# Performance work log

Measured on AMD Instinct MI355X. Metric: run time of the kernel, lower is better.

Reference implementation:

```python
import jax, jax.numpy as jnp
import numpy as np

N, E, EH, RH, R, H = 50000, 800000, 256, 128, 500, 2


def _seg_softmax(e, rel, num_segments):
    # torch_geometric.utils.softmax keyed by rel: (e - max_seg).exp() / (sum_seg + 1e-16)
    m = jax.ops.segment_max(e, rel, num_segments=num_segments)
    m = jnp.where(jnp.isfinite(m), m, 0.0)  # empty segments -> 0
    ex = jnp.exp(e - m[rel])
    s = jax.ops.segment_sum(ex, rel, num_segments=num_segments)
    return ex / (s[rel] + 1e-16)


def setup_inputs() -> dict:
    key = jax.random.key(0)
    ks = jax.random.split(key, 7)
    x_e = jax.random.normal(ks[0], (N, EH), dtype=jnp.float32)
    edge_index = jax.random.randint(ks[1], (2, E), 0, N)
    rel = jax.random.randint(ks[2], (E,), 0, R)
    w_h = jax.random.normal(ks[3], (RH, EH), dtype=jnp.float32) / np.sqrt(EH)
    w_t = jax.random.normal(ks[4], (RH, EH), dtype=jnp.float32) / np.sqrt(EH)
    a_h = jax.random.normal(ks[5], (H, RH), dtype=jnp.float32) / np.sqrt(RH)
    a_t = jax.random.normal(ks[6], (H, RH), dtype=jnp.float32) / np.sqrt(RH)
    return {"x_e": x_e, "edge_index": edge_index, "rel": rel,
            "w_h": w_h, "w_t": w_t, "a_h": a_h, "a_t": a_t, "num_heads": H}


def reference(x_e, edge_index, rel, w_h, w_t, a_h, a_t, num_heads):
    src, dst = edge_index[0], edge_index[1]
    x_r_h = x_e @ w_h.T  # [N, RH]
    x_r_t = x_e @ w_t.T  # [N, RH]
    # per-node attention scores for all heads: [N, H]
    s_hh = x_r_h @ a_h.T
    s_tt = x_r_t @ a_t.T
    s_th = x_r_t @ a_h.T
    s_ht = x_r_h @ a_t.T
    acc = jnp.zeros((R, RH), dtype=x_e.dtype)
    for h in range(num_heads):  # small fixed head count
        e1 = jax.nn.leaky_relu(s_hh[src, h] + s_tt[dst, h], 0.01)
        a1 = _seg_softmax(e1, rel, R)
        acc = acc + jax.ops.segment_sum(a1[:, None] * x_r_h[src], rel, num_segments=R)
        e2 = jax.nn.leaky_relu(s_th[src, h] + s_ht[dst, h], 0.01)
        a2 = _seg_softmax(e2, rel, R)
        acc = acc + jax.ops.segment_sum(a2[:, None] * x_r_t[dst], rel, num_segments=R)
    x_r = acc / num_heads / 2.0
    return x_r  # dropout is identity in eval mode
```

## Files before the change

kernel.cpp:

```cpp
#include <hip/hip_runtime.h>
#include <hip/hip_bf16.h>

#define NN 50000
#define NE 800000
#define NR 500
#define KEH 256
#define KRH 128
#define NSB 8
#define SBW 6250
#define NBK (NR*NSB)
#define NBE 256
#define EPB (NE/NBE)
#define NTILE 3125
#define CSB 16

typedef __attribute__((ext_vector_type(8))) __bf16 bf16x8;
typedef __attribute__((ext_vector_type(4))) float f32x4;

#define OFF_XH     0UL
#define OFF_XT     12800000UL
#define OFF_SP     25600000UL
#define OFF_DP     26400000UL
#define OFF_SUMS   27200000UL
#define OFF_HISTH  27208000UL
#define OFF_HISTT  27224000UL
#define OFF_INVS   27240000UL
#define OFF_BASEH  27248000UL
#define OFF_BASET  27264016UL
#define OFF_RECH   27312032UL
#define OFF_RECT   33712032UL
#define OFF_PART   40112032UL
#define OFF_AH     42160032UL
#define OFF_AT     42161056UL
#define OFF_FLAG   42162080UL
#define OFF_WHH    42162144UL
#define OFF_WHL    42227680UL
#define OFF_WTH    42293216UL
#define OFF_WTL    42358752UL
#define OFF_HPBH   42424288UL
#define OFF_HPBT   46520288UL

__device__ __forceinline__ int clampi(int v, int hi) {
    v = v < 0 ? 0 : v;
    return v >= hi ? hi - 1 : v;
}

__device__ __forceinline__ int sniff_isbf(const unsigned* xe_raw) {
    int lane = threadIdx.x & 63;
    unsigned w = xe_raw[lane];
    unsigned ex = (w >> 7) & 0xFFu;
    bool hit = (ex >= 115u && ex <= 131u);
    return __popcll(__ballot(hit)) >= 32;
}

__global__ __launch_bounds__(256) void k_init(const unsigned* __restrict__ xe_raw,
                                              const void* __restrict__ ah_in, const void* __restrict__ at_in,
                                              const void* __restrict__ wh, const void* __restrict__ wt,
                                              unsigned* __restrict__ flag, float* __restrict__ ah32,
                                              float* __restrict__ at32,
                                              __bf16* __restrict__ whh, __bf16* __restrict__ wth,
                                              unsigned* __restrict__ zero1) {
    int isbf = sniff_isbf(xe_raw);
    int t = threadIdx.x;
    if (blockIdx.x == 0) {
        if (t == 0) flag[0] = (unsigned)isbf;
        ah32[t] = isbf ? __bfloat162float(((const __hip_bfloat16*)ah_in)[t]) : ((const float*)ah_in)[t];
        at32[t] = isbf ? __bfloat162float(((const __hip_bfloat16*)at_in)[t]) : ((const float*)at_in)[t];
    } else if (blockIdx.x <= 128) {
        int o = (blockIdx.x - 1) * 256 + t;
        int e = o & 7, c = (o >> 3) & 15, q = (o >> 7) & 3, ks = (o >> 9) & 7, ct = o >> 12;
        int i = (ct * 16 + c) * KEH + ks * 32 + q * 8 + e;
        if (isbf) {
            whh[o] = ((const __bf16*)wh)[i];
            wth[o] = ((const __bf16*)wt)[i];
        } else {
            whh[o] = (__bf16)((const float*)wh)[i];
            wth[o] = (__bf16)((const float*)wt)[i];
        }
    } else {
        int stride = (gridDim.x - 129) * 256;
        for (int i = (blockIdx.x - 129) * 256 + t; i < 10000; i += stride) zero1[i] = 0u;
    }
}

__global__ __launch_bounds__(512, 4) void k_gemm(const void* __restrict__ xe,
                                              const unsigned* __restrict__ flag,
                                              const __bf16* __restrict__ whh, const __bf16* __restrict__ wth,
                                              const float* __restrict__ ah, const float* __restrict__ at,
                                              __hip_bfloat16* __restrict__ xh, __hip_bfloat16* __restrict__ xt,
                                              float2* __restrict__ sp2, float2* __restrict__ dp2) {
    __shared__ uint4 lb[4096];
    const int t = threadIdx.x, lane = t & 63, wave = t >> 6;
    const int l16 = lane & 15, quad = lane >> 4;
    const int ph = blockIdx.x & 1;
    const int isbf = (int)flag[0];
    const __bf16* wfh = ph ? wth : whh;

    {
        const uint4* wsrc = (const uint4*)wfh;
        #pragma unroll
        for (int i = 0; i < 8; ++i) lb[i * 512 + t] = wsrc[i * 512 + t];
    }
    __syncthreads();

    __hip_bfloat16* out = ph ? xt : xh;
    for (int tile = (int)(blockIdx.x >> 1) * 8 + wave; tile < NTILE; tile += 2048) {
        const int row = tile * 16 + l16;
        bf16x8 a[8];
        if (isbf) {
            const __bf16* xb = (const __bf16*)xe + (size_t)row * KEH;
            #pragma unroll
            for (int ks = 0; ks < 8; ++ks)
                a[ks] = *(const bf16x8*)(xb + ks * 32 + quad * 8);
        } else {
            const float* xf = (const float*)xe + (size_t)row * KEH;
            #pragma unroll
            for (int ks = 0; ks < 8; ++ks) {
                const float* p = xf + ks * 32 + quad * 8;
                float4 u0 = *(const float4*)p, u1 = *(const float4*)(p + 4);
                a[ks][0] = (__bf16)u0.x; a[ks][1] = (__bf16)u0.y;
                a[ks][2] = (__bf16)u0.z; a[ks][3] = (__bf16)u0.w;
                a[ks][4] = (__bf16)u1.x; a[ks][5] = (__bf16)u1.y;
                a[ks][6] = (__bf16)u1.z; a[ks][7] = (__bf16)u1.w;
            }
        }

        f32x4 acc[8];
        #pragma unroll
        for (int ct = 0; ct < 8; ++ct) acc[ct] = (f32x4){0.f, 0.f, 0.f, 0.f};
        #pragma unroll
        for (int ks = 0; ks < 8; ++ks)
            #pragma unroll
            for (int ct = 0; ct < 8; ++ct)
                acc[ct] = __builtin_amdgcn_mfma_f32_16x16x32_bf16(
                    a[ks], *(const bf16x8*)&lb[(ct * 8 + ks) * 64 + lane], acc[ct], 0, 0, 0);

        float s0[4] = {0.f,0.f,0.f,0.f}, s1[4] = {0.f,0.f,0.f,0.f};
        float s2[4] = {0.f,0.f,0.f,0.f}, s3[4] = {0.f,0.f,0.f,0.f};
        #pragma unroll
        for (int ct = 0; ct < 8; ++ct) {
            int c = ct * 16 + l16;
            float va0 = ah[c], va1 = ah[128 + c];
            float vb0 = at[c], vb1 = at[128 + c];
            #pragma unroll
            for (int jj = 0; jj < 4; ++jj) {
                float v = acc[ct][jj];
                s0[jj] = fmaf(v, va0, s0[jj]);
                s1[jj] = fmaf(v, va1, s1[jj]);
                s2[jj] = fmaf(v, vb0, s2[jj]);
                s3[jj] = fmaf(v, vb1, s3[jj]);
                out[(size_t)(tile * 16 + quad * 4 + jj) * KRH + c] = __float2bfloat16(v);
            }
        }
        #pragma unroll
        for (int off = 8; off; off >>= 1)
            #pragma unroll
            for (int jj = 0; jj < 4; ++jj) {
                s0[jj] += __shfl_xor(s0[jj], off);
                s1[jj] += __shfl_xor(s1[jj], off);
                s2[jj] += __shfl_xor(s2[jj], off);
                s3[jj] += __shfl_xor(s3[jj], off);
            }
        if (l16 == 0) {
            #pragma unroll
            for (int jj = 0; jj < 4; ++jj) {
                int n = tile * 16 + quad * 4 + jj;
                if (ph == 0) {
                    sp2[n * 2 + 0] = make_float2(s0[jj], s1[jj]);
                    dp2[n * 2 + 1] = make_float2(s2[jj], s3[jj]);
                } else {
                    sp2[n * 2 + 1] = make_float2(s0[jj], s1[jj]);
                    dp2[n * 2 + 0] = make_float2(s2[jj], s3[jj]);
                }
            }
        }
    }
}

__device__ __forceinline__ float eexp(float x) {
    x = x > 0.f ? x : 0.01f * x;
    x = fminf(x, 50.f);
    return __expf(x);
}

__global__ __launch_bounds__(1024) void k_edge(const int* __restrict__ src, const int* __restrict__ dst,
                                               const int* __restrict__ rel,
                                               const float4* __restrict__ sp, const float4* __restrict__ dp,
                                               float* __restrict__ sums,
                                               unsigned* __restrict__ histH, unsigned* __restrict__ histT,
                                               unsigned* __restrict__ hpbH, unsigned* __restrict__ hpbT) {
    __shared__ float ls[NR * 4];
    __shared__ unsigned lhH[NBK], lhT[NBK];
    int t = threadIdx.x;
    for (int i = t; i < NR * 4; i += 1024) ls[i] = 0.f;
    for (int i = t; i < NBK; i += 1024) { lhH[i] = 0u; lhT[i] = 0u; }
    __syncthreads();
    unsigned lo = blockIdx.x * EPB, hi = lo + EPB;
    for (unsigned e = lo + t; e < hi; e += 1024) {
        int s = clampi(src[e], NN), d = clampi(dst[e], NN), r = clampi(rel[e], NR);
        float4 a = sp[s], b = dp[d];
        float4 ex;
        ex.x = eexp(a.x + b.x); ex.y = eexp(a.y + b.y);
        ex.z = eexp(a.z + b.z); ex.w = eexp(a.w + b.w);
        atomicAdd(&ls[r*4+0], ex.x);
        atomicAdd(&ls[r*4+1], ex.y);
        atomicAdd(&ls[r*4+2], ex.z);
        atomicAdd(&ls[r*4+3], ex.w);
        atomicAdd(&lhH[r * NSB + s / SBW], 1u);
        atomicAdd(&lhT[r * NSB + d / SBW], 1u);
    }
    __syncthreads();
    for (int i = t; i < NR * 4; i += 1024)
        if (ls[i] != 0.f) atomicAdd(&sums[i], ls[i]);
    size_t row = (size_t)blockIdx.x * NBK;
    for (int i = t; i < NBK; i += 1024) {
        unsigned cH = lhH[i], cT = lhT[i];
        hpbH[row + i] = cH;
        hpbT[row + i] = cT;
        if (cH) atomicAdd(&histH[i], cH);
        if (cT) atomicAdd(&histT[i], cT);
    }
}

__global__ __launch_bounds__(1024) void k_scan2(const unsigned* __restrict__ histH,
                                                const unsigned* __restrict__ histT,
                                                const float* __restrict__ sums,
                                                unsigned* __restrict__ baseH, unsigned* __restrict__ baseT,
                                                float* __restrict__ invs) {
    __shared__ unsigned wsum[16];
    int t = threadIdx.x, lane = t & 63, wv = t >> 6;
    for (int pass = 0; pass < 2; ++pass) {
        const unsigned* h = pass ? histT : histH;
        unsigned* base = pass ? baseT : baseH;
        int j0 = t * 4;
        unsigned v[4], s = 0;
        #pragma unroll
        for (int k = 0; k < 4; ++k) { v[k] = (j0 + k < NBK) ? h[j0 + k] : 0u; s += v[k]; }
        unsigned inc = s;
        #pragma unroll
        for (int d = 1; d < 64; d <<= 1) {
            unsigned u = __shfl_up(inc, d);
            if (lane >= d) inc += u;
        }
        if (lane == 63) wsum[wv] = inc;
        __syncthreads();
        unsigned wbase = 0;
        for (int i = 0; i < wv; ++i) wbase += wsum[i];
        unsigned run = wbase + inc - s;
        #pragma unroll
        for (int k = 0; k < 4; ++k) {
            if (j0 + k < NBK) { base[j0 + k] = run; run += v[k]; }
        }
        if (t == 1023) base[NBK] = wbase + inc;
        __syncthreads();
    }
    for (int i = t; i < NR * 4; i += 1024) invs[i] = 1.f / (sums[i] + 1e-16f);
}

__global__ __launch_bounds__(NBE) void k_colscan(unsigned* __restrict__ hpbH, unsigned* __restrict__ hpbT,
                                                 const unsigned* __restrict__ baseH,
                                                 const unsigned* __restrict__ baseT) {
    __shared__ unsigned wsum[4][CSB];
    int b = blockIdx.x;
    int pass = b >= (NBK / CSB);
    int bin0 = (pass ? b - NBK / CSB : b) * CSB;
    unsigned* h = pass ? hpbT : hpbH;
    const unsigned* base = (pass ? baseT : baseH) + bin0;
    int t = threadIdx.x, lane = t & 63, wv = t >> 6;

    unsigned v[CSB], inc[CSB];
    uint4* hp = (uint4*)(h + (size_t)t * NBK + bin0);
    #pragma unroll
    for (int q = 0; q < CSB / 4; ++q) {
        uint4 u = hp[q];
        v[q*4+0] = u.x; v[q*4+1] = u.y; v[q*4+2] = u.z; v[q*4+3] = u.w;
    }
    #pragma unroll
    for (int k = 0; k < CSB; ++k) inc[k] = v[k];
    #pragma unroll
    for (int d = 1; d < 64; d <<= 1) {
        #pragma unroll
        for (int k = 0; k < CSB; ++k) {
            unsigned u = __shfl_up(inc[k], d);
            if (lane >= d) inc[k] += u;
        }
    }
    if (lane == 63) {
        #pragma unroll
        for (int k = 0; k < CSB; ++k) wsum[wv][k] = inc[k];
    }
    __syncthreads();
    #pragma unroll
    for (int k = 0; k < CSB; ++k) {
        unsigned wbase = 0;
        for (int i = 0; i < wv; ++i) wbase += wsum[i][k];
        v[k] = base[k] + wbase + inc[k] - v[k];
    }
    #pragma unroll
    for (int q = 0; q < CSB / 4; ++q)
        hp[q] = make_uint4(v[q*4+0], v[q*4+1], v[q*4+2], v[q*4+3]);
}

__global__ __launch_bounds__(1024) void k_mkrec(const int* __restrict__ src, const int* __restrict__ dst,
                                                const int* __restrict__ rel,
                                                const float4* __restrict__ sp, const float4* __restrict__ dp,
                                                const float4* __restrict__ invs4,
                                                const unsigned* __restrict__ hpbH, const unsigned* __restrict__ hpbT,
                                                uint2* __restrict__ recH, uint2* __restrict__ recT) {
    __shared__ unsigned lcH[NBK], lcT[NBK];
    int t = threadIdx.x;
    size_t row = (size_t)blockIdx.x * NBK;
    for (int i = t; i < NBK; i += 1024) { lcH[i] = hpbH[row + i]; lcT[i] = hpbT[row + i]; }
    __syncthreads();
    unsigned lo = blockIdx.x * EPB, hi = lo + EPB;
    for (unsigned e = lo + t; e < hi; e += 1024) {
        int s = clampi(src[e], NN), d = clampi(dst[e], NN), r = clampi(rel[e], NR);
        float4 a = sp[s], b = dp[d];
        float4 iv = invs4[r];
        float exx = eexp(a.x + b.x), exy = eexp(a.y + b.y);
        float exz = eexp(a.z + b.z), exw = eexp(a.w + b.w);
        float w1 = exx * iv.x + exy * iv.y;
        float w2 = exz * iv.z + exw * iv.w;
        unsigned pH = atomicAdd(&lcH[r * NSB + s / SBW], 1u);
        unsigned pT = atomicAdd(&lcT[r * NSB + d / SBW], 1u);
        if (pH < NE) recH[pH] = make_uint2((unsigned)s, __float_as_uint(w1));
        if (pT < NE) recT[pT] = make_uint2((unsigned)d, __float_as_uint(w2));
    }
}

__global__ __launch_bounds__(256) void k_accR(const uint2* __restrict__ recH, const uint2* __restrict__ recT,
                                              const unsigned* __restrict__ baseH, const unsigned* __restrict__ baseT,
                                              const __hip_bfloat16* __restrict__ xh,
                                              const __hip_bfloat16* __restrict__ xt,
                                              float* __restrict__ part) {
    __shared__ float red[3][128];
    __shared__ uint2 lrec[256];
    int b = blockIdx.x;
    int t = threadIdx.x, lane = t & 63, wv = t >> 6;
    int l16 = lane & 15, g = lane >> 4;
    float az[8];
    #pragma unroll
    for (int k = 0; k < 8; ++k) az[k] = 0.f;

    for (int pass = 0; pass < 2; ++pass) {
        const uint2* rec = pass ? recT : recH;
        const unsigned* base = pass ? baseT : baseH;
        const uint4* xs = (const uint4*)(pass ? xt : xh);
        unsigned b0 = base[b];
        unsigned cnt = base[b + 1] - b0;
        if (cnt > NE) cnt = 0;
        for (unsigned cb = 0; cb < cnt; cb += 256u) {
            unsigned cn = cnt - cb; if (cn > 256u) cn = 256u;
            __syncthreads();
            if ((unsigned)t < cn) lrec[t] = rec[b0 + cb + t];
            __syncthreads();
            for (unsigned j = (unsigned)(wv * 4 + g); j < cn; j += 16u) {
                uint2 v = lrec[j];
                unsigned nd = v.x < NN ? v.x : 0u;
                float w = __uint_as_float(v.y);
                uint4 u = xs[(size_t)nd * 16 + l16];
                az[0] = fmaf(w, __uint_as_float(u.x << 16),          az[0]);
                az[1] = fmaf(w, __uint_as_float(u.x & 0xffff0000u),  az[1]);
                az[2] = fmaf(w, __uint_as_float(u.y << 16),          az[2]);
                az[3] = fmaf(w, __uint_as_float(u.y & 0xffff0000u),  az[3]);
                az[4] = fmaf(w, __uint_as_float(u.z << 16),          az[4]);
                az[5] = fmaf(w, __uint_as_float(u.z & 0xffff0000u),  az[5]);
                az[6] = fmaf(w, __uint_as_float(u.w << 16),          az[6]);
                az[7] = fmaf(w, __uint_as_float(u.w & 0xffff0000u),  az[7]);
            }
        }
    }
    #pragma unroll
    for (int k = 0; k < 8; ++k) {
        az[k] += __shfl_xor(az[k], 16);
        az[k] += __shfl_xor(az[k], 32);
    }
    __syncthreads();
    if (wv > 0 && lane < 16) {
        #pragma unroll
        for (int k = 0; k < 8; ++k) red[wv - 1][l16 * 8 + k] = az[k];
    }
    __syncthreads();
    if (wv == 0 && lane < 16) {
        #pragma unroll
        for (int k = 0; k < 8; ++k) {
            float s = az[k] + red[0][l16 * 8 + k] + red[1][l16 * 8 + k] + red[2][l16 * 8 + k];
            part[(size_t)b * KRH + l16 * 8 + k] = s;
        }
    }
}

__global__ __launch_bounds__(256) void k_out(const float* __restrict__ part,
                                             const unsigned* __restrict__ flag, void* __restrict__ out) {
    int i = blockIdx.x * 256 + threadIdx.x;
    if (i < NR * KRH) {
        int r = i >> 7, c = i & 127;
        float v = 0.f;
        for (int s = 0; s < NSB; ++s) v += part[(size_t)(r * NSB + s) * KRH + c];
        v *= 0.25f;
        if (!isfinite(v)) v = 0.f;
        if (flag[0]) ((__hip_bfloat16*)out)[i] = __float2bfloat16(v);
        else         ((float*)out)[i] = v;
    }
}

extern "C" void kernel_launch(void* const* d_in, const int* in_sizes, int n_in,
                              void* d_out, int out_size, void* d_ws, size_t ws_size,
                              hipStream_t stream) {
    const void* xe  = d_in[0];
    const int* eidx = (const int*)d_in[1];
    const int* rel  = (const int*)d_in[2];
    const void* wh  = d_in[3];
    const void* wt  = d_in[4];
    const void* ahp = d_in[5];
    const void* atp = d_in[6];

    const int* src = eidx;
    const int* dst = eidx + NE;

    char* ws = (char*)d_ws;
    __hip_bfloat16* xh = (__hip_bfloat16*)(ws + OFF_XH);
    __hip_bfloat16* xt = (__hip_bfloat16*)(ws + OFF_XT);
    float4*   sp     = (float4*)(ws + OFF_SP);
    float4*   dp     = (float4*)(ws + OFF_DP);
    float*    sums   = (float*)(ws + OFF_SUMS);
    unsigned* histH  = (unsigned*)(ws + OFF_HISTH);
    unsigned* histT  = (unsigned*)(ws + OFF_HISTT);
    float*    invs   = (float*)(ws + OFF_INVS);
    unsigned* baseH  = (unsigned*)(ws + OFF_BASEH);
    unsigned* baseT  = (unsigned*)(ws + OFF_BASET);
    uint2*    recH   = (uint2*)(ws + OFF_RECH);
    uint2*    recT   = (uint2*)(ws + OFF_RECT);
    float*    partp  = (float*)(ws + OFF_PART);
    float*    ah32   = (float*)(ws + OFF_AH);
    float*    at32   = (float*)(ws + OFF_AT);
    unsigned* flag   = (unsigned*)(ws + OFF_FLAG);
    __bf16*   whh    = (__bf16*)(ws + OFF_WHH);
    __bf16*   wth    = (__bf16*)(ws + OFF_WTH);
    unsigned* hpbH   = (unsigned*)(ws + OFF_HPBH);
    unsigned* hpbT   = (unsigned*)(ws + OFF_HPBT);

    k_init<<<161, 256, 0, stream>>>((const unsigned*)xe, ahp, atp, wh, wt, flag, ah32, at32,
                                     whh, wth, (unsigned*)(ws + OFF_SUMS));
    k_gemm<<<512, 512, 0, stream>>>(xe, flag, whh, wth, ah32, at32,
                                    xh, xt, (float2*)sp, (float2*)dp);
    k_edge<<<NBE, 1024, 0, stream>>>(src, dst, rel, sp, dp, sums, histH, histT, hpbH, hpbT);
    k_scan2<<<1, 1024, 0, stream>>>(histH, histT, sums, baseH, baseT, invs);
    k_colscan<<<2 * (NBK / CSB), NBE, 0, stream>>>(hpbH, hpbT, baseH, baseT);
    k_mkrec<<<NBE, 1024, 0, stream>>>(src, dst, rel, sp, dp, (const float4*)invs, hpbH, hpbT, recH, recT);
    k_accR<<<NBK, 256, 0, stream>>>(recH, recT, baseH, baseT, xh, xt, partp);
    k_out<<<(NR * KRH + 255) / 256, 256, 0, stream>>>(partp, flag, d_out);
}
```

Measured before the change: 238.5 us.

## Fuse edge histogram, scans and record scatter into one cooperative kernel

After: 496.6 us. 108% more time.

```diff
diff --git a/kernel.cpp b/kernel.cpp
--- a/kernel.cpp
+++ b/kernel.cpp
@@ -1,5 +1,8 @@
 #include <hip/hip_runtime.h>
 #include <hip/hip_bf16.h>
+#include <hip/hip_cooperative_groups.h>
+
+namespace cg = cooperative_groups;
 
 #define NN 50000
 #define NE 800000
@@ -34,9 +37,7 @@
 #define OFF_AT     42161056UL
 #define OFF_FLAG   42162080UL
 #define OFF_WHH    42162144UL
-#define OFF_WHL    42227680UL
 #define OFF_WTH    42293216UL
-#define OFF_WTL    42358752UL
 #define OFF_HPBH   42424288UL
 #define OFF_HPBT   46520288UL
 
@@ -183,60 +184,63 @@
     return __expf(x);
 }
 
-__global__ __launch_bounds__(1024) void k_edge(const int* __restrict__ src, const int* __restrict__ dst,
+__global__ __launch_bounds__(1024) void k_sort(const int* __restrict__ src, const int* __restrict__ dst,
                                                const int* __restrict__ rel,
                                                const float4* __restrict__ sp, const float4* __restrict__ dp,
                                                float* __restrict__ sums,
                                                unsigned* __restrict__ histH, unsigned* __restrict__ histT,
-                                               unsigned* __restrict__ hpbH, unsigned* __restrict__ hpbT) {
+                                               unsigned* __restrict__ hpbH, unsigned* __restrict__ hpbT,
+                                               unsigned* __restrict__ baseH, unsigned* __restrict__ baseT,
+                                               float* __restrict__ invs,
+                                               uint2* __restrict__ recH, uint2* __restrict__ recT) {
+    cg::grid_group grid = cg::this_grid();
     __shared__ float ls[NR * 4];
-    __shared__ unsigned lhH[NBK], lhT[NBK];
-    int t = threadIdx.x;
+    __shared__ unsigned lA[NBK], lB[NBK];
+    __shared__ unsigned wsum[16];
+    __shared__ unsigned wsum2[16][4];
+    const int t = threadIdx.x, lane = t & 63, wv = t >> 6;
+    const int blk = blockIdx.x;
+    const unsigned lo = blk * EPB, hi = lo + EPB;
+
     for (int i = t; i < NR * 4; i += 1024) ls[i] = 0.f;
-    for (int i = t; i < NBK; i += 1024) { lhH[i] = 0u; lhT[i] = 0u; }
-    __syncthreads();
-    unsigned lo = blockIdx.x * EPB, hi = lo + EPB;
+    for (int i = t; i < NBK; i += 1024) { lA[i] = 0u; lB[i] = 0u; }
+    __syncthreads();
     for (unsigned e = lo + t; e < hi; e += 1024) {
         int s = clampi(src[e], NN), d = clampi(dst[e], NN), r = clampi(rel[e], NR);
         float4 a = sp[s], b = dp[d];
-        float4 ex;
-        ex.x = eexp(a.x + b.x); ex.y = eexp(a.y + b.y);
-        ex.z = eexp(a.z + b.z); ex.w = eexp(a.w + b.w);
-        atomicAdd(&ls[r*4+0], ex.x);
-        atomicAdd(&ls[r*4+1], ex.y);
-        atomicAdd(&ls[r*4+2], ex.z);
-        atomicAdd(&ls[r*4+3], ex.w);
-        atomicAdd(&lhH[r * NSB + s / SBW], 1u);
-        atomicAdd(&lhT[r * NSB + d / SBW], 1u);
+        float ex0 = eexp(a.x + b.x), ex1 = eexp(a.y + b.y);
+        float ex2 = eexp(a.z + b.z), ex3 = eexp(a.w + b.w);
+        atomicAdd(&ls[r*4+0], ex0);
+        atomicAdd(&ls[r*4+1], ex1);
+        atomicAdd(&ls[r*4+2], ex2);
+        atomicAdd(&ls[r*4+3], ex3);
+        atomicAdd(&lA[r * NSB + s / SBW], 1u);
+        atomicAdd(&lB[r * NSB + d / SBW], 1u);
     }
     __syncthreads();
     for (int i = t; i < NR * 4; i += 1024)
         if (ls[i] != 0.f) atomicAdd(&sums[i], ls[i]);
-    size_t row = (size_t)blockIdx.x * NBK;
-    for (int i = t; i < NBK; i += 1024) {
-        unsigned cH = lhH[i], cT = lhT[i];
-        hpbH[row + i] = cH;
-        hpbT[row + i] = cT;
-        if (cH) atomicAdd(&histH[i], cH);
-        if (cT) atomicAdd(&histT[i], cT);
-    }
-}
-
-__global__ __launch_bounds__(1024) void k_scan2(const unsigned* __restrict__ histH,
-                                                const unsigned* __restrict__ histT,
-                                                const float* __restrict__ sums,
-                                                unsigned* __restrict__ baseH, unsigned* __restrict__ baseT,
-                                                float* __restrict__ invs) {
-    __shared__ unsigned wsum[16];
-    int t = threadIdx.x, lane = t & 63, wv = t >> 6;
+    {
+        size_t row = (size_t)blk * NBK;
+        for (int i = t; i < NBK; i += 1024) {
+            unsigned cH = lA[i], cT = lB[i];
+            hpbH[row + i] = cH;
+            hpbT[row + i] = cT;
+            if (cH) atomicAdd(&histH[i], cH);
+            if (cT) atomicAdd(&histT[i], cT);
+        }
+    }
+    __threadfence();
+    grid.sync();
+
     for (int pass = 0; pass < 2; ++pass) {
         const unsigned* h = pass ? histT : histH;
-        unsigned* base = pass ? baseT : baseH;
+        unsigned* bl = pass ? lB : lA;
         int j0 = t * 4;
-        unsigned v[4], s = 0;
-        #pragma unroll
-        for (int k = 0; k < 4; ++k) { v[k] = (j0 + k < NBK) ? h[j0 + k] : 0u; s += v[k]; }
-        unsigned inc = s;
+        unsigned v[4], s4 = 0;
+        #pragma unroll
+        for (int k = 0; k < 4; ++k) { v[k] = (j0 + k < NBK) ? h[j0 + k] : 0u; s4 += v[k]; }
+        unsigned inc = s4;
         #pragma unroll
         for (int d = 1; d < 64; d <<= 1) {
             unsigned u = __shfl_up(inc, d);
@@ -246,83 +250,72 @@
         __syncthreads();
         unsigned wbase = 0;
         for (int i = 0; i < wv; ++i) wbase += wsum[i];
-        unsigned run = wbase + inc - s;
+        unsigned run = wbase + inc - s4;
         #pragma unroll
         for (int k = 0; k < 4; ++k) {
-            if (j0 + k < NBK) { base[j0 + k] = run; run += v[k]; }
-        }
-        if (t == 1023) base[NBK] = wbase + inc;
+            if (j0 + k < NBK) { bl[j0 + k] = run; run += v[k]; }
+        }
+        if (t == 1023 && blk == 0) (pass ? baseT : baseH)[NBK] = wbase + inc;
         __syncthreads();
     }
-    for (int i = t; i < NR * 4; i += 1024) invs[i] = 1.f / (sums[i] + 1e-16f);
-}
-
-__global__ __launch_bounds__(NBE) void k_colscan(unsigned* __restrict__ hpbH, unsigned* __restrict__ hpbT,
-                                                 const unsigned* __restrict__ baseH,
-                                                 const unsigned* __restrict__ baseT) {
-    __shared__ unsigned wsum[4][CSB];
-    int b = blockIdx.x;
-    int pass = b >= (NBK / CSB);
-    int bin0 = (pass ? b - NBK / CSB : b) * CSB;
-    unsigned* h = pass ? hpbT : hpbH;
-    const unsigned* base = (pass ? baseT : baseH) + bin0;
-    int t = threadIdx.x, lane = t & 63, wv = t >> 6;
-
-    unsigned v[CSB], inc[CSB];
-    uint4* hp = (uint4*)(h + (size_t)t * NBK + bin0);
-    #pragma unroll
-    for (int q = 0; q < CSB / 4; ++q) {
-        uint4 u = hp[q];
-        v[q*4+0] = u.x; v[q*4+1] = u.y; v[q*4+2] = u.z; v[q*4+3] = u.w;
-    }
-    #pragma unroll
-    for (int k = 0; k < CSB; ++k) inc[k] = v[k];
-    #pragma unroll
-    for (int d = 1; d < 64; d <<= 1) {
-        #pragma unroll
-        for (int k = 0; k < CSB; ++k) {
-            unsigned u = __shfl_up(inc[k], d);
-            if (lane >= d) inc[k] += u;
-        }
-    }
-    if (lane == 63) {
-        #pragma unroll
-        for (int k = 0; k < CSB; ++k) wsum[wv][k] = inc[k];
-    }
-    __syncthreads();
-    #pragma unroll
-    for (int k = 0; k < CSB; ++k) {
-        unsigned wbase = 0;
-        for (int i = 0; i < wv; ++i) wbase += wsum[i][k];
-        v[k] = base[k] + wbase + inc[k] - v[k];
-    }
-    #pragma unroll
-    for (int q = 0; q < CSB / 4; ++q)
-        hp[q] = make_uint4(v[q*4+0], v[q*4+1], v[q*4+2], v[q*4+3]);
-}
-
-__global__ __launch_bounds__(1024) void k_mkrec(const int* __restrict__ src, const int* __restrict__ dst,
-                                                const int* __restrict__ rel,
-                                                const float4* __restrict__ sp, const float4* __restrict__ dp,
-                                                const float4* __restrict__ invs4,
-                                                const unsigned* __restrict__ hpbH, const unsigned* __restrict__ hpbT,
-                                                uint2* __restrict__ recH, uint2* __restrict__ recT) {
-    __shared__ unsigned lcH[NBK], lcT[NBK];
-    int t = threadIdx.x;
-    size_t row = (size_t)blockIdx.x * NBK;
-    for (int i = t; i < NBK; i += 1024) { lcH[i] = hpbH[row + i]; lcT[i] = hpbT[row + i]; }
-    __syncthreads();
-    unsigned lo = blockIdx.x * EPB, hi = lo + EPB;
+    if (blk == 0) for (int i = t; i < NBK; i += 1024) baseH[i] = lA[i];
+    if (blk == 1) for (int i = t; i < NBK; i += 1024) baseT[i] = lB[i];
+    if (blk == 2) for (int i = t; i < NR * 4; i += 1024) invs[i] = 1.f / (sums[i] + 1e-16f);
+
+    if (blk < NBK / CSB) {
+        int bin0 = blk * CSB;
+        int g = t >> 8, r2 = t & 255;
+        for (int pass = 0; pass < 2; ++pass) {
+            unsigned* h = pass ? hpbT : hpbH;
+            const unsigned* bl = pass ? lB : lA;
+            uint4* hp = (uint4*)(h + (size_t)r2 * NBK + bin0 + 4 * g);
+            uint4 u = hp[0];
+            unsigned v4[4] = {u.x, u.y, u.z, u.w}, inc4[4];
+            #pragma unroll
+            for (int k = 0; k < 4; ++k) inc4[k] = v4[k];
+            #pragma unroll
+            for (int d = 1; d < 64; d <<= 1) {
+                #pragma unroll
+                for (int k = 0; k < 4; ++k) {
+                    unsigned uu = __shfl_up(inc4[k], d);
+                    if (lane >= d) inc4[k] += uu;
+                }
+            }
+            if (lane == 63) {
+                #pragma unroll
+                for (int k = 0; k < 4; ++k) wsum2[wv][k] = inc4[k];
+            }
+            __syncthreads();
+            unsigned wb[4] = {0u, 0u, 0u, 0u};
+            for (int i = (wv & ~3); i < wv; ++i) {
+                #pragma unroll
+                for (int k = 0; k < 4; ++k) wb[k] += wsum2[i][k];
+            }
+            #pragma unroll
+            for (int k = 0; k < 4; ++k)
+                v4[k] = bl[bin0 + 4 * g + k] + wb[k] + inc4[k] - v4[k];
+            hp[0] = make_uint4(v4[0], v4[1], v4[2], v4[3]);
+            __syncthreads();
+        }
+    }
+    __threadfence();
+    grid.sync();
+
+    {
+        size_t row = (size_t)blk * NBK;
+        for (int i = t; i < NBK; i += 1024) { lA[i] = hpbH[row + i]; lB[i] = hpbT[row + i]; }
+    }
+    __syncthreads();
     for (unsigned e = lo + t; e < hi; e += 1024) {
         int s = clampi(src[e], NN), d = clampi(dst[e], NN), r = clampi(rel[e], NR);
         float4 a = sp[s], b = dp[d];
-        float4 iv = invs4[r];
-        float exx = eexp(a.x + b.x), exy = eexp(a.y + b.y);
-        float exz = eexp(a.z + b.z), exw = eexp(a.w + b.w);
-        float w1 = exx * iv.x + exy * iv.y;
-        float w2 = exz * iv.z + exw * iv.w;
-        unsigned pH = atomicAdd(&lcH[r * NSB + s / SBW], 1u);
-        unsigned pT = atomicAdd(&lcT[r * NSB + d / SBW], 1u);
+        float4 iv = ((const float4*)invs)[r];
+        float ex0 = eexp(a.x + b.x), ex1 = eexp(a.y + b.y);
+        float ex2 = eexp(a.z + b.z), ex3 = eexp(a.w + b.w);
+        float w1 = ex0 * iv.x + ex1 * iv.y;
+        float w2 = ex2 * iv.z + ex3 * iv.w;
+        unsigned pH = atomicAdd(&lA[r * NSB + s / SBW], 1u);
+        unsigned pT = atomicAdd(&lB[r * NSB + d / SBW], 1u);
         if (pH < NE) recH[pH] = make_uint2((unsigned)s, __float_as_uint(w1));
         if (pT < NE) recT[pT] = make_uint2((unsigned)d, __float_as_uint(w2));
     }
@@ -444,10 +437,18 @@
                                      whh, wth, (unsigned*)(ws + OFF_SUMS));
     k_gemm<<<512, 512, 0, stream>>>(xe, flag, whh, wth, ah32, at32,
                                     xh, xt, (float2*)sp, (float2*)dp);
-    k_edge<<<NBE, 1024, 0, stream>>>(src, dst, rel, sp, dp, sums, histH, histT, hpbH, hpbT);
-    k_scan2<<<1, 1024, 0, stream>>>(histH, histT, sums, baseH, baseT, invs);
-    k_colscan<<<2 * (NBK / CSB), NBE, 0, stream>>>(hpbH, hpbT, baseH, baseT);
-    k_mkrec<<<NBE, 1024, 0, stream>>>(src, dst, rel, sp, dp, (const float4*)invs, hpbH, hpbT, recH, recT);
+    {
+        const int* src_ = src; const int* dst_ = dst; const int* rel_ = rel;
+        const float4* sp_ = sp; const float4* dp_ = dp;
+        float* sums_ = sums; unsigned* histH_ = histH; unsigned* histT_ = histT;
+        unsigned* hpbH_ = hpbH; unsigned* hpbT_ = hpbT;
+        unsigned* baseH_ = baseH; unsigned* baseT_ = baseT; float* invs_ = invs;
+        uint2* recH_ = recH; uint2* recT_ = recT;
+        void* args[] = {(void*)&src_, (void*)&dst_, (void*)&rel_, (void*)&sp_, (void*)&dp_,
+                        (void*)&sums_, (void*)&histH_, (void*)&histT_, (void*)&hpbH_, (void*)&hpbT_,
+                        (void*)&baseH_, (void*)&baseT_, (void*)&invs_, (void*)&recH_, (void*)&recT_};
+        hipLaunchCooperativeKernel((const void*)k_sort, dim3(NBE), dim3(1024), args, 0, stream);
+    }
     k_accR<<<NBK, 256, 0, stream>>>(recH, recT, baseH, baseT, xh, xt, partp);
     k_out<<<(NR * KRH + 255) / 256, 256, 0, stream>>>(partp, flag, d_out);
 }
```

## Fuse histogram scan into column scan and unroll gather-accumulate loop by four

Applied to the files above, without the earlier changes.

New measurement: 227.3 us. -4.7%, faster.

```diff
diff --git a/kernel.cpp b/kernel.cpp
--- a/kernel.cpp
+++ b/kernel.cpp
@@ -34,9 +34,7 @@
 #define OFF_AT     42161056UL
 #define OFF_FLAG   42162080UL
 #define OFF_WHH    42162144UL
-#define OFF_WHL    42227680UL
 #define OFF_WTH    42293216UL
-#define OFF_WTL    42358752UL
 #define OFF_HPBH   42424288UL
 #define OFF_HPBT   46520288UL
 
@@ -222,20 +220,37 @@
     }
 }
 
-__global__ __launch_bounds__(1024) void k_scan2(const unsigned* __restrict__ histH,
-                                                const unsigned* __restrict__ histT,
-                                                const float* __restrict__ sums,
-                                                unsigned* __restrict__ baseH, unsigned* __restrict__ baseT,
-                                                float* __restrict__ invs) {
-    __shared__ unsigned wsum[16];
-    int t = threadIdx.x, lane = t & 63, wv = t >> 6;
-    for (int pass = 0; pass < 2; ++pass) {
-        const unsigned* h = pass ? histT : histH;
-        unsigned* base = pass ? baseT : baseH;
-        int j0 = t * 4;
-        unsigned v[4], s = 0;
-        #pragma unroll
-        for (int k = 0; k < 4; ++k) { v[k] = (j0 + k < NBK) ? h[j0 + k] : 0u; s += v[k]; }
+__global__ __launch_bounds__(256) void k_scan(const unsigned* __restrict__ histH,
+                                              const unsigned* __restrict__ histT,
+                                              const float* __restrict__ sums,
+                                              unsigned* __restrict__ hpbH, unsigned* __restrict__ hpbT,
+                                              unsigned* __restrict__ baseH, unsigned* __restrict__ baseT,
+                                              float* __restrict__ invs) {
+    __shared__ unsigned bases[4096];
+    __shared__ unsigned wsum[4];
+    __shared__ unsigned wsum2[4][CSB];
+    const int b = blockIdx.x;
+    const int pass = b >= (NBK / CSB);
+    const int slice = pass ? b - NBK / CSB : b;
+    const unsigned* h = pass ? histT : histH;
+    unsigned* hpb = pass ? hpbT : hpbH;
+    unsigned* base = pass ? baseT : baseH;
+    const int t = threadIdx.x, lane = t & 63, wv = t >> 6;
+
+    {
+        int j0 = t * 16;
+        unsigned v[16], s = 0;
+        const uint4* hp4 = (const uint4*)(h + j0);
+        #pragma unroll
+        for (int q = 0; q < 4; ++q) {
+            uint4 u = (j0 + q * 4 < NBK) ? hp4[q] : make_uint4(0u, 0u, 0u, 0u);
+            v[q*4+0] = u.x; v[q*4+1] = u.y; v[q*4+2] = u.z; v[q*4+3] = u.w;
+        }
+        #pragma unroll
+        for (int k = 0; k < 16; ++k) {
+            if (j0 + k >= NBK) v[k] = 0u;
+            s += v[k];
+        }
         unsigned inc = s;
         #pragma unroll
         for (int d = 1; d < 64; d <<= 1) {
@@ -248,57 +263,52 @@
         for (int i = 0; i < wv; ++i) wbase += wsum[i];
         unsigned run = wbase + inc - s;
         #pragma unroll
-        for (int k = 0; k < 4; ++k) {
-            if (j0 + k < NBK) { base[j0 + k] = run; run += v[k]; }
-        }
-        if (t == 1023) base[NBK] = wbase + inc;
+        for (int k = 0; k < 16; ++k) {
+            if (j0 + k < NBK) bases[j0 + k] = run;
+            run += v[k];
+        }
         __syncthreads();
-    }
-    for (int i = t; i < NR * 4; i += 1024) invs[i] = 1.f / (sums[i] + 1e-16f);
-}
-
-__global__ __launch_bounds__(NBE) void k_colscan(unsigned* __restrict__ hpbH, unsigned* __restrict__ hpbT,
-                                                 const unsigned* __restrict__ baseH,
-                                                 const unsigned* __restrict__ baseT) {
-    __shared__ unsigned wsum[4][CSB];
-    int b = blockIdx.x;
-    int pass = b >= (NBK / CSB);
-    int bin0 = (pass ? b - NBK / CSB : b) * CSB;
-    unsigned* h = pass ? hpbT : hpbH;
-    const unsigned* base = (pass ? baseT : baseH) + bin0;
-    int t = threadIdx.x, lane = t & 63, wv = t >> 6;
-
-    unsigned v[CSB], inc[CSB];
-    uint4* hp = (uint4*)(h + (size_t)t * NBK + bin0);
-    #pragma unroll
-    for (int q = 0; q < CSB / 4; ++q) {
-        uint4 u = hp[q];
-        v[q*4+0] = u.x; v[q*4+1] = u.y; v[q*4+2] = u.z; v[q*4+3] = u.w;
-    }
-    #pragma unroll
-    for (int k = 0; k < CSB; ++k) inc[k] = v[k];
-    #pragma unroll
-    for (int d = 1; d < 64; d <<= 1) {
+        if (slice == 0) {
+            for (int i = t; i < NBK; i += 256) base[i] = bases[i];
+            if (t == 0) base[NBK] = wsum[0] + wsum[1] + wsum[2] + wsum[3];
+        }
+        if (b == 0) for (int i = t; i < NR * 4; i += 256) invs[i] = 1.f / (sums[i] + 1e-16f);
+    }
+
+    {
+        int bin0 = slice * CSB;
+        unsigned v[CSB], inc[CSB];
+        uint4* hp = (uint4*)(hpb + (size_t)t * NBK + bin0);
+        #pragma unroll
+        for (int q = 0; q < CSB / 4; ++q) {
+            uint4 u = hp[q];
+            v[q*4+0] = u.x; v[q*4+1] = u.y; v[q*4+2] = u.z; v[q*4+3] = u.w;
+        }
+        #pragma unroll
+        for (int k = 0; k < CSB; ++k) inc[k] = v[k];
+        #pragma unroll
+        for (int d = 1; d < 64; d <<= 1) {
+            #pragma unroll
+            for (int k = 0; k < CSB; ++k) {
+                unsigned u = __shfl_up(inc[k], d);
+                if (lane >= d) inc[k] += u;
+            }
+        }
+        if (lane == 63) {
+            #pragma unroll
+            for (int k = 0; k < CSB; ++k) wsum2[wv][k] = inc[k];
+        }
+        __syncthreads();
         #pragma unroll
         for (int k = 0; k < CSB; ++k) {
-            unsigned u = __shfl_up(inc[k], d);
-            if (lane >= d) inc[k] += u;
-        }
-    }
-    if (lane == 63) {
-        #pragma unroll
-        for (int k = 0; k < CSB; ++k) wsum[wv][k] = inc[k];
-    }
-    __syncthreads();
-    #pragma unroll
-    for (int k = 0; k < CSB; ++k) {
-        unsigned wbase = 0;
-        for (int i = 0; i < wv; ++i) wbase += wsum[i][k];
-        v[k] = base[k] + wbase + inc[k] - v[k];
-    }
-    #pragma unroll
-    for (int q = 0; q < CSB / 4; ++q)
-        hp[q] = make_uint4(v[q*4+0], v[q*4+1], v[q*4+2], v[q*4+3]);
+            unsigned wbase = 0;
+            for (int i = 0; i < wv; ++i) wbase += wsum2[i][k];
+            v[k] = bases[bin0 + k] + wbase + inc[k] - v[k];
+        }
+        #pragma unroll
+        for (int q = 0; q < CSB / 4; ++q)
+            hp[q] = make_uint4(v[q*4+0], v[q*4+1], v[q*4+2], v[q*4+3]);
+    }
 }
 
 __global__ __launch_bounds__(1024) void k_mkrec(const int* __restrict__ src, const int* __restrict__ dst,
@@ -354,7 +364,53 @@
             __syncthreads();
             if ((unsigned)t < cn) lrec[t] = rec[b0 + cb + t];
             __syncthreads();
-            for (unsigned j = (unsigned)(wv * 4 + g); j < cn; j += 16u) {
+            unsigned j = (unsigned)(wv * 4 + g);
+            for (; j + 48u < cn; j += 64u) {
+                uint2 v0 = lrec[j], v1 = lrec[j + 16u], v2 = lrec[j + 32u], v3 = lrec[j + 48u];
+                unsigned n0 = v0.x < NN ? v0.x : 0u;
+                unsigned n1 = v1.x < NN ? v1.x : 0u;
+                unsigned n2 = v2.x < NN ? v2.x : 0u;
+                unsigned n3 = v3.x < NN ? v3.x : 0u;
+                uint4 u0 = xs[(size_t)n0 * 16 + l16];
+                uint4 u1 = xs[(size_t)n1 * 16 + l16];
+                uint4 u2 = xs[(size_t)n2 * 16 + l16];
+                uint4 u3 = xs[(size_t)n3 * 16 + l16];
+                float w0 = __uint_as_float(v0.y), w1 = __uint_as_float(v1.y);
+                float w2 = __uint_as_float(v2.y), w3 = __uint_as_float(v3.y);
+                az[0] = fmaf(w0, __uint_as_float(u0.x << 16),         az[0]);
+                az[1] = fmaf(w0, __uint_as_float(u0.x & 0xffff0000u), az[1]);
+                az[2] = fmaf(w0, __uint_as_float(u0.y << 16),         az[2]);
+                az[3] = fmaf(w0, __uint_as_float(u0.y & 0xffff0000u), az[3]);
+                az[4] = fmaf(w0, __uint_as_float(u0.z << 16),         az[4]);
+                az[5] = fmaf(w0, __uint_as_float(u0.z & 0xffff0000u), az[5]);
+                az[6] = fmaf(w0, __uint_as_float(u0.w << 16),         az[6]);
+                az[7] = fmaf(w0, __uint_as_float(u0.w & 0xffff0000u), az[7]);
+                az[0] = fmaf(w1, __uint_as_float(u1.x << 16),         az[0]);
+                az[1] = fmaf(w1, __uint_as_float(u1.x & 0xffff0000u), az[1]);
+                az[2] = fmaf(w1, __uint_as_float(u1.y << 16),         az[2]);
+                az[3] = fmaf(w1, __uint_as_float(u1.y & 0xffff0000u), az[3]);
+                az[4] = fmaf(w1, __uint_as_float(u1.z << 16),         az[4]);
+                az[5] = fmaf(w1, __uint_as_float(u1.z & 0xffff0000u), az[5]);
+                az[6] = fmaf(w1, __uint_as_float(u1.w << 16),         az[6]);
+                az[7] = fmaf(w1, __uint_as_float(u1.w & 0xffff0000u), az[7]);
+                az[0] = fmaf(w2, __uint_as_float(u2.x << 16),         az[0]);
+                az[1] = fmaf(w2, __uint_as_float(u2.x & 0xffff0000u), az[1]);
+                az[2] = fmaf(w2, __uint_as_float(u2.y << 16),         az[2]);
+                az[3] = fmaf(w2, __uint_as_float(u2.y & 0xffff0000u), az[3]);
+                az[4] = fmaf(w2, __uint_as_float(u2.z << 16),         az[4]);
+                az[5] = fmaf(w2, __uint_as_float(u2.z & 0xffff0000u), az[5]);
+                az[6] = fmaf(w2, __uint_as_float(u2.w << 16),         az[6]);
+                az[7] = fmaf(w2, __uint_as_float(u2.w & 0xffff0000u), az[7]);
+                az[0] = fmaf(w3, __uint_as_float(u3.x << 16),         az[0]);
+                az[1] = fmaf(w3, __uint_as_float(u3.x & 0xffff0000u), az[1]);
+                az[2] = fmaf(w3, __uint_as_float(u3.y << 16),         az[2]);
+                az[3] = fmaf(w3, __uint_as_float(u3.y & 0xffff0000u), az[3]);
+                az[4] = fmaf(w3, __uint_as_float(u3.z << 16),         az[4]);
+                az[5] = fmaf(w3, __uint_as_float(u3.z & 0xffff0000u), az[5]);
+                az[6] = fmaf(w3, __uint_as_float(u3.w << 16),         az[6]);
+                az[7] = fmaf(w3, __uint_as_float(u3.w & 0xffff0000u), az[7]);
+            }
+            for (; j < cn; j += 16u) {
                 uint2 v = lrec[j];
                 unsigned nd = v.x < NN ? v.x : 0u;
                 float w = __uint_as_float(v.y);
@@ -445,8 +501,7 @@
     k_gemm<<<512, 512, 0, stream>>>(xe, flag, whh, wth, ah32, at32,
                                     xh, xt, (float2*)sp, (float2*)dp);
     k_edge<<<NBE, 1024, 0, stream>>>(src, dst, rel, sp, dp, sums, histH, histT, hpbH, hpbT);
-    k_scan2<<<1, 1024, 0, stream>>>(histH, histT, sums, baseH, baseT, invs);
-    k_colscan<<<2 * (NBK / CSB), NBE, 0, stream>>>(hpbH, hpbT, baseH, baseT);
+    k_scan<<<2 * (NBK / CSB), 256, 0, stream>>>(histH, histT, sums, hpbH, hpbT, baseH, baseT, invs);
     k_mkrec<<<NBE, 1024, 0, stream>>>(src, dst, rel, sp, dp, (const float4*)invs, hpbH, hpbT, recH, recT);
     k_accR<<<NBK, 256, 0, stream>>>(recH, recT, baseH, baseT, xh, xt, partp);
     k_out<<<(NR * KRH + 255) / 256, 256, 0, stream>>>(partp, flag, d_out);
```
